# Kernel tuning notes

Measured on AMD Instinct MI355X. Metric: run time of the kernel, lower is better.

Reference implementation:

```python
import jax, jax.numpy as jnp
import numpy as np

D_MODEL = 1024
D_FF = 1024
NUM_EXPERTS = 8
TOP_K = 2


def setup_inputs() -> dict:
    key = jax.random.key(0)
    ks = jax.random.split(key, 5)
    s_in = 1.0 / np.sqrt(D_MODEL)
    s_ff = 1.0 / np.sqrt(D_FF)
    return {
        "x": jax.random.normal(ks[0], (4, 2048, D_MODEL), dtype=jnp.float32),
        "gate_w": jax.random.normal(ks[1], (NUM_EXPERTS, D_MODEL), dtype=jnp.float32) * s_in,
        # torch Linear weight layout: [out_features, in_features], stacked over experts
        "w_gate": jax.random.normal(ks[2], (NUM_EXPERTS, D_FF, D_MODEL), dtype=jnp.float32) * s_in,
        "w_up": jax.random.normal(ks[3], (NUM_EXPERTS, D_FF, D_MODEL), dtype=jnp.float32) * s_in,
        "w_down": jax.random.normal(ks[4], (NUM_EXPERTS, D_MODEL, D_FF), dtype=jnp.float32) * s_ff,
    }


def reference(x, gate_w, w_gate, w_up, w_down):
    B, S, D = x.shape
    T = B * S
    E = gate_w.shape[0]
    xt = x.reshape(T, D)

    # Router
    logits = xt @ gate_w.T                      # [T, E]
    probs = jax.nn.softmax(logits, axis=-1)
    top_v, top_i = jax.lax.top_k(probs, TOP_K)  # [T, K]
    top_v = top_v / jnp.sum(top_v, axis=-1, keepdims=True)

    tokens_per_expert = jnp.sum(jax.nn.one_hot(top_i, E, dtype=jnp.float32), axis=(0, 1))  # [E]
    f = tokens_per_expert / jnp.sum(tokens_per_expert)
    P = jnp.mean(probs, axis=0)
    aux_loss = E * jnp.sum(f * P)

    # Combine weights: per-token weight for each expert (sum over top-k slots)
    combine = jnp.zeros((T, E), dtype=x.dtype).at[jnp.arange(T)[:, None], top_i].add(top_v)  # [T, E]

    # Dense per-expert SwiGLU (equivalent math to masked gather/scatter loop)
    g = jnp.einsum('td,efd->etf', xt, w_gate)   # [E, T, F]
    u = jnp.einsum('td,efd->etf', xt, w_up)     # [E, T, F]
    act = jax.nn.silu(g) * u
    eo = jnp.einsum('etf,edf->etd', act, w_down)  # [E, T, D]

    out = jnp.einsum('te,etd->td', combine, eo).reshape(B, S, D)
    return out, aux_loss, tokens_per_expert
```

## Files before the change

kernel.cpp:

```cpp
#include <hip/hip_runtime.h>


#define T_TOK   8192
#define DM      1024
#define DFF     1024
#define NE      8
#define CAP     16384
#define R1_BLK  (T_TOK / 4)

typedef __attribute__((ext_vector_type(8))) short bf16x8;
typedef __attribute__((ext_vector_type(4))) float f32x4;

#define ASYNC16(gp, lp) __builtin_amdgcn_global_load_lds( \
    (const __attribute__((address_space(1))) unsigned int*)(gp), \
    (__attribute__((address_space(3))) unsigned int*)(lp), 16, 0, 0)

__device__ __forceinline__ unsigned short f2bf(float f) {
    union { float f; unsigned u; } c; c.f = f;
    unsigned r = c.u + 0x7fffu + ((c.u >> 16) & 1u);
    return (unsigned short)(r >> 16);
}

__global__ __launch_bounds__(256) void cvt_kernel(const float* __restrict__ src,
                                                  unsigned short* __restrict__ dst, int n) {
    int i = (blockIdx.x * 256 + threadIdx.x) * 4;
    if (i >= n) return;
    float4 v = *(const float4*)(src + i);
    ushort4 o;
    o.x = f2bf(v.x); o.y = f2bf(v.y); o.z = f2bf(v.z); o.w = f2bf(v.w);
    *(ushort4*)(dst + i) = o;
}

__global__ __launch_bounds__(256) void router_kernel(
    const float* __restrict__ x, const float* __restrict__ gate_w,
    unsigned short* __restrict__ xb,
    int* __restrict__ topi, float2* __restrict__ topw,
    float* __restrict__ psum_part)
{
    __shared__ float gw[NE * DM];
    __shared__ float blk_psum[NE];
    int tid = threadIdx.x;
    for (int i = tid; i < NE * DM; i += 256) gw[i] = gate_w[i];
    if (tid < NE) blk_psum[tid] = 0.f;
    __syncthreads();

    int wv = tid >> 6, lane = tid & 63;
    int t = blockIdx.x * 4 + wv;

    float acc[NE];
    #pragma unroll
    for (int e = 0; e < NE; ++e) acc[e] = 0.f;
    const float* xr = x + (size_t)t * DM;
    unsigned short* xbr = xb + (size_t)t * DM;
    #pragma unroll 4
    for (int i = 0; i < DM / 64; ++i) {
        float xv = xr[i * 64 + lane];
        xbr[i * 64 + lane] = f2bf(xv);
        #pragma unroll
        for (int e = 0; e < NE; ++e)
            acc[e] += xv * gw[e * DM + i * 64 + lane];
    }
    #pragma unroll
    for (int e = 0; e < NE; ++e) {
        float v = acc[e];
        #pragma unroll
        for (int s = 32; s > 0; s >>= 1) v += __shfl_xor(v, s, 64);
        acc[e] = v;
    }
    if (lane == 0) {
        float mx = acc[0];
        #pragma unroll
        for (int e = 1; e < NE; ++e) mx = fmaxf(mx, acc[e]);
        float p[NE], sum = 0.f;
        #pragma unroll
        for (int e = 0; e < NE; ++e) { p[e] = expf(acc[e] - mx); sum += p[e]; }
        float inv = 1.f / sum;
        #pragma unroll
        for (int e = 0; e < NE; ++e) { p[e] *= inv; atomicAdd(&blk_psum[e], p[e]); }
        int i1 = 0; float v1 = p[0];
        #pragma unroll
        for (int e = 1; e < NE; ++e) if (p[e] > v1) { v1 = p[e]; i1 = e; }
        int i2 = -1; float v2 = -1.f;
        #pragma unroll
        for (int e = 0; e < NE; ++e) { if (e == i1) continue; if (p[e] > v2) { v2 = p[e]; i2 = e; } }
        float winv = 1.f / (v1 + v2);
        topi[t] = i1 | (i2 << 8);
        topw[t] = make_float2(v1 * winv, v2 * winv);
    }
    __syncthreads();
    if (tid < NE) psum_part[blockIdx.x * NE + tid] = blk_psum[tid];
}

__global__ __launch_bounds__(256) void scatter_kernel(
    const int* __restrict__ topi, const float2* __restrict__ topw,
    int* __restrict__ elist, float* __restrict__ wlist, int* __restrict__ ecnt)
{
    __shared__ int lcnt[NE];
    __shared__ int lbase[NE];
    int tid = threadIdx.x;
    if (tid < NE) lcnt[tid] = 0;
    __syncthreads();
    int t = blockIdx.x * 256 + tid;
    int pk = topi[t];
    float2 w = topw[t];
    int e1 = pk & 0xff, e2 = (pk >> 8) & 0xff;
    int p1 = atomicAdd(&lcnt[e1], 1);
    int p2 = atomicAdd(&lcnt[e2], 1);
    __syncthreads();
    if (tid < NE) lbase[tid] = atomicAdd(&ecnt[tid], lcnt[tid]);
    __syncthreads();
    int o1 = lbase[e1] + p1;
    elist[e1 * CAP + o1] = t * 2 + 0;
    wlist[e1 * CAP + o1] = w.x;
    int o2 = lbase[e2] + p2;
    elist[e2 * CAP + o2] = t * 2 + 1;
    wlist[e2 * CAP + o2] = w.y;
}

__global__ __launch_bounds__(256) void finalize_kernel(
    const int* __restrict__ ecnt, const float* __restrict__ psum_part,
    float* __restrict__ out_tail)
{
    __shared__ float red[256];
    __shared__ float parts[NE];
    int tid = threadIdx.x;
    int e = tid & 7, b0 = tid >> 3;
    float s = 0.f;
    for (int b = b0; b < R1_BLK; b += 32) s += psum_part[b * NE + e];
    red[tid] = s;
    __syncthreads();
    if (tid < NE) {
        float tot = 0.f;
        #pragma unroll
        for (int j = 0; j < 32; ++j) tot += red[tid + NE * j];
        float P = tot / (float)T_TOK;
        float f = (float)ecnt[tid] / (float)(2 * T_TOK);
        parts[tid] = f * P;
        out_tail[1 + tid] = (float)ecnt[tid];
    }
    __syncthreads();
    if (tid == 0) {
        float s2 = 0.f;
        for (int i = 0; i < NE; ++i) s2 += parts[i];
        out_tail[0] = (float)NE * s2;
    }
}

__global__ __launch_bounds__(256) void gemm1_kernel(
    const unsigned short* __restrict__ xb,
    const unsigned short* __restrict__ wgb,
    const unsigned short* __restrict__ wub,
    const int* __restrict__ elist, const int* __restrict__ ecnt,
    unsigned short* __restrict__ Hbuf)
{
    int e = blockIdx.z, mt = blockIdx.y, ft = blockIdx.x;
    int ne = ecnt[e];
    if (mt * 128 >= ne) return;

    __shared__ unsigned short As[128 * 64];
    __shared__ unsigned short Gs[64 * 64];
    __shared__ unsigned short Us[64 * 64];
    __shared__ int tsafe[128];
    __shared__ int rawts[128];

    int tid = threadIdx.x;
    if (tid < 128) {
        int pos = mt * 128 + tid;
        int ts0 = elist[e * CAP + mt * 128];
        int ts = (pos < ne) ? elist[e * CAP + pos] : ts0;
        tsafe[tid] = ts >> 1;
        rawts[tid] = (pos < ne) ? ts : -1;
    }
    __syncthreads();

    int wave = tid >> 6, lane = tid & 63;
    int quad = lane >> 4, col = lane & 15;
    int cr = tid >> 3;
    int cl = ((tid & 7) ^ (cr & 7)) * 8;

    const size_t woff = (size_t)e * (size_t)DFF * DM;
    const unsigned short* ap[4];
    #pragma unroll
    for (int j = 0; j < 4; ++j) ap[j] = xb + (size_t)tsafe[j * 32 + cr] * DM + cl;
    const unsigned short* gp[2];
    const unsigned short* up[2];
    #pragma unroll
    for (int j = 0; j < 2; ++j) {
        gp[j] = wgb + woff + (size_t)(ft * 64 + j * 32 + cr) * DM + cl;
        up[j] = wub + woff + (size_t)(ft * 64 + j * 32 + cr) * DM + cl;
    }
    unsigned short* lA = As + wave * 512;
    unsigned short* lG = Gs + wave * 512;
    unsigned short* lU = Us + wave * 512;

    f32x4 accG[2][4], accU[2][4];
    #pragma unroll
    for (int i = 0; i < 2; ++i)
        #pragma unroll
        for (int n = 0; n < 4; ++n) { accG[i][n] = (f32x4){0,0,0,0}; accU[i][n] = (f32x4){0,0,0,0}; }

    for (int k0 = 0; k0 < DM; k0 += 64) {
        __syncthreads();
        #pragma unroll
        for (int j = 0; j < 4; ++j) ASYNC16(ap[j] + k0, lA + j * 2048);
        #pragma unroll
        for (int j = 0; j < 2; ++j) {
            ASYNC16(gp[j] + k0, lG + j * 2048);
            ASYNC16(up[j] + k0, lU + j * 2048);
        }
        __syncthreads();
        #pragma unroll
        for (int ksoff = 0; ksoff < 8; ksoff += 4) {
            bf16x8 a[2], g[4], u[4];
            #pragma unroll
            for (int i = 0; i < 2; ++i) {
                int m = wave * 32 + i * 16 + col;
                a[i] = *(const bf16x8*)&As[m * 64 + ((quad + ksoff) ^ (m & 7)) * 8];
            }
            #pragma unroll
            for (int n = 0; n < 4; ++n) {
                int nb = n * 16 + col;
                int off = nb * 64 + ((quad + ksoff) ^ (nb & 7)) * 8;
                g[n] = *(const bf16x8*)&Gs[off];
                u[n] = *(const bf16x8*)&Us[off];
            }
            #pragma unroll
            for (int i = 0; i < 2; ++i)
                #pragma unroll
                for (int n = 0; n < 4; ++n) {
                    accG[i][n] = __builtin_amdgcn_mfma_f32_16x16x32_bf16(a[i], g[n], accG[i][n], 0, 0, 0);
                    accU[i][n] = __builtin_amdgcn_mfma_f32_16x16x32_bf16(a[i], u[n], accU[i][n], 0, 0, 0);
                }
        }
    }
    #pragma unroll
    for (int i = 0; i < 2; ++i) {
        #pragma unroll
        for (int r = 0; r < 4; ++r) {
            int row = wave * 32 + i * 16 + quad * 4 + r;
            int ts = rawts[row];
            if (ts < 0) continue;
            unsigned short* hr = Hbuf + (size_t)ts * DFF + ft * 64 + col;
            #pragma unroll
            for (int n = 0; n < 4; ++n) {
                float gg = accG[i][n][r], uu = accU[i][n][r];
                float h = (gg / (1.f + expf(-gg))) * uu;
                hr[n * 16] = f2bf(h);
            }
        }
    }
}

__global__ __launch_bounds__(256) void gemm2_kernel(
    const unsigned short* __restrict__ Hbuf,
    const unsigned short* __restrict__ wdb,
    const int* __restrict__ elist, const float* __restrict__ wlist,
    const int* __restrict__ ecnt, float* __restrict__ out)
{
    int e = blockIdx.z, mt = blockIdx.y, dt = blockIdx.x;
    int ne = ecnt[e];
    if (mt * 128 >= ne) return;

    __shared__ unsigned short As[128 * 64];
    __shared__ unsigned short Bs[128 * 64];
    __shared__ int tsafe[128];
    __shared__ int rawts[128];
    __shared__ float wrow[128];

    int tid = threadIdx.x;
    if (tid < 128) {
        int pos = mt * 128 + tid;
        int ts0 = elist[e * CAP + mt * 128];
        int ts = (pos < ne) ? elist[e * CAP + pos] : ts0;
        tsafe[tid] = ts;
        rawts[tid] = (pos < ne) ? ts : -1;
        wrow[tid] = (pos < ne) ? wlist[e * CAP + pos] : 0.f;
    }
    __syncthreads();

    int wave = tid >> 6, lane = tid & 63;
    int quad = lane >> 4, col = lane & 15;
    int wr = (wave >> 1) * 64, wc = (wave & 1) * 64;
    int cr = tid >> 3;
    int cl = ((tid & 7) ^ (cr & 7)) * 8;

    const size_t woff = (size_t)e * (size_t)DM * DFF;
    const unsigned short* ap[4];
    const unsigned short* bp[4];
    #pragma unroll
    for (int j = 0; j < 4; ++j) {
        ap[j] = Hbuf + (size_t)tsafe[j * 32 + cr] * DFF + cl;
        bp[j] = wdb + woff + (size_t)(dt * 128 + j * 32 + cr) * DFF + cl;
    }
    unsigned short* lA = As + wave * 512;
    unsigned short* lB = Bs + wave * 512;

    f32x4 acc[4][4];
    #pragma unroll
    for (int i = 0; i < 4; ++i)
        #pragma unroll
        for (int n = 0; n < 4; ++n) acc[i][n] = (f32x4){0,0,0,0};

    for (int k0 = 0; k0 < DFF; k0 += 64) {
        __syncthreads();
        #pragma unroll
        for (int j = 0; j < 4; ++j) {
            ASYNC16(ap[j] + k0, lA + j * 2048);
            ASYNC16(bp[j] + k0, lB + j * 2048);
        }
        __syncthreads();
        #pragma unroll
        for (int ksoff = 0; ksoff < 8; ksoff += 4) {
            bf16x8 a[4], b[4];
            #pragma unroll
            for (int i = 0; i < 4; ++i) {
                int m = wr + i * 16 + col;
                a[i] = *(const bf16x8*)&As[m * 64 + ((quad + ksoff) ^ (m & 7)) * 8];
            }
            #pragma unroll
            for (int n = 0; n < 4; ++n) {
                int nb = wc + n * 16 + col;
                b[n] = *(const bf16x8*)&Bs[nb * 64 + ((quad + ksoff) ^ (nb & 7)) * 8];
            }
            #pragma unroll
            for (int i = 0; i < 4; ++i)
                #pragma unroll
                for (int n = 0; n < 4; ++n)
                    acc[i][n] = __builtin_amdgcn_mfma_f32_16x16x32_bf16(a[i], b[n], acc[i][n], 0, 0, 0);
        }
    }
    #pragma unroll
    for (int i = 0; i < 4; ++i) {
        #pragma unroll
        for (int r = 0; r < 4; ++r) {
            int row = wr + i * 16 + quad * 4 + r;
            int ts = rawts[row];
            if (ts < 0) continue;
            int t = ts >> 1;
            float w = wrow[row];
            float* orow = out + (size_t)t * DM + dt * 128 + wc + col;
            #pragma unroll
            for (int n = 0; n < 4; ++n)
                atomicAdd(orow + n * 16, w * acc[i][n][r]);
        }
    }
}

extern "C" void kernel_launch(void* const* d_in, const int* in_sizes, int n_in,
                              void* d_out, int out_size, void* d_ws, size_t ws_size,
                              hipStream_t stream) {
    const float* x      = (const float*)d_in[0];
    const float* gate_w = (const float*)d_in[1];
    const float* w_gate = (const float*)d_in[2];
    const float* w_up   = (const float*)d_in[3];
    const float* w_down = (const float*)d_in[4];
    float* out = (float*)d_out;

    char* p = (char*)d_ws;
    unsigned short* xb   = (unsigned short*)p; p += (size_t)T_TOK * DM * 2;
    unsigned short* wgb  = (unsigned short*)p; p += (size_t)NE * DFF * DM * 2;
    unsigned short* wub  = (unsigned short*)p; p += (size_t)NE * DFF * DM * 2;
    unsigned short* wdb  = (unsigned short*)p; p += (size_t)NE * DM * DFF * 2;
    unsigned short* Hbuf = (unsigned short*)p; p += (size_t)2 * T_TOK * DFF * 2;
    int*   elist = (int*)p;   p += (size_t)NE * CAP * 4;
    float* wlist = (float*)p; p += (size_t)NE * CAP * 4;
    int*   ecnt  = (int*)p;   p += NE * 4;
    int*   topi  = (int*)p;   p += (size_t)T_TOK * 4;
    float2* topw = (float2*)p; p += (size_t)T_TOK * 8;
    float* psum_part = (float*)p; p += (size_t)R1_BLK * NE * 4;

    hipMemsetAsync(d_out, 0, (size_t)out_size * 4, stream);
    hipMemsetAsync(ecnt, 0, NE * 4, stream);

    const int nW = NE * DFF * DM;
    cvt_kernel<<<(nW / 4 + 255) / 256, 256, 0, stream>>>(w_gate, wgb, nW);
    cvt_kernel<<<(nW / 4 + 255) / 256, 256, 0, stream>>>(w_up, wub, nW);
    cvt_kernel<<<(nW / 4 + 255) / 256, 256, 0, stream>>>(w_down, wdb, nW);

    router_kernel<<<R1_BLK, 256, 0, stream>>>(x, gate_w, xb, topi, topw, psum_part);
    scatter_kernel<<<T_TOK / 256, 256, 0, stream>>>(topi, topw, elist, wlist, ecnt);
    finalize_kernel<<<1, 256, 0, stream>>>(ecnt, psum_part, out + (size_t)T_TOK * DM);

    gemm1_kernel<<<dim3(DFF / 64, CAP / 128, NE), 256, 0, stream>>>(xb, wgb, wub, elist, ecnt, Hbuf);
    gemm2_kernel<<<dim3(DM / 128, CAP / 128, NE), 256, 0, stream>>>(Hbuf, wdb, elist, wlist, ecnt, out);
}
```

Measured before the change: 381.0 us.

## Replace atomic scatter-add in down-projection with bf16 staging and combine kernel

The down-projection GEMM now writes each token-slot's expert output as bf16 into a staging buffer (reusing the converted gate-weight buffer) instead of weighted float atomicAdds into the output. A new combine kernel reads both slots per token and writes the weighted sum directly, which also removes the output memset and the per-expert weight list. The three weight-conversion launches are merged into one kernel. This trades global atomic contention for an extra launch and a bf16 round-trip of expert outputs, which adds some precision loss.

```diff
diff --git a/kernel.cpp b/kernel.cpp
--- a/kernel.cpp
+++ b/kernel.cpp
@@ -20,15 +20,24 @@
     unsigned r = c.u + 0x7fffu + ((c.u >> 16) & 1u);
     return (unsigned short)(r >> 16);
 }
-
-__global__ __launch_bounds__(256) void cvt_kernel(const float* __restrict__ src,
-                                                  unsigned short* __restrict__ dst, int n) {
-    int i = (blockIdx.x * 256 + threadIdx.x) * 4;
-    if (i >= n) return;
-    float4 v = *(const float4*)(src + i);
+__device__ __forceinline__ float bf2f(unsigned short h) {
+    union { unsigned u; float f; } c; c.u = ((unsigned)h) << 16;
+    return c.f;
+}
+
+__global__ __launch_bounds__(256) void cvt3_kernel(
+    const float* __restrict__ s0, const float* __restrict__ s1, const float* __restrict__ s2,
+    unsigned short* __restrict__ d0, unsigned short* __restrict__ d1, unsigned short* __restrict__ d2)
+{
+    int idx = blockIdx.x * 256 + threadIdx.x;
+    int seg = idx >> 21;
+    int off = (idx & ((1 << 21) - 1)) * 4;
+    const float* s = (seg == 0) ? s0 : (seg == 1) ? s1 : s2;
+    unsigned short* d = (seg == 0) ? d0 : (seg == 1) ? d1 : d2;
+    float4 v = *(const float4*)(s + off);
     ushort4 o;
     o.x = f2bf(v.x); o.y = f2bf(v.y); o.z = f2bf(v.z); o.w = f2bf(v.w);
-    *(ushort4*)(dst + i) = o;
+    *(ushort4*)(d + off) = o;
 }
 
 __global__ __launch_bounds__(256) void router_kernel(
@@ -92,8 +101,8 @@
 }
 
 __global__ __launch_bounds__(256) void scatter_kernel(
-    const int* __restrict__ topi, const float2* __restrict__ topw,
-    int* __restrict__ elist, float* __restrict__ wlist, int* __restrict__ ecnt)
+    const int* __restrict__ topi,
+    int* __restrict__ elist, int* __restrict__ ecnt)
 {
     __shared__ int lcnt[NE];
     __shared__ int lbase[NE];
@@ -102,19 +111,14 @@
     __syncthreads();
     int t = blockIdx.x * 256 + tid;
     int pk = topi[t];
-    float2 w = topw[t];
     int e1 = pk & 0xff, e2 = (pk >> 8) & 0xff;
     int p1 = atomicAdd(&lcnt[e1], 1);
     int p2 = atomicAdd(&lcnt[e2], 1);
     __syncthreads();
     if (tid < NE) lbase[tid] = atomicAdd(&ecnt[tid], lcnt[tid]);
     __syncthreads();
-    int o1 = lbase[e1] + p1;
-    elist[e1 * CAP + o1] = t * 2 + 0;
-    wlist[e1 * CAP + o1] = w.x;
-    int o2 = lbase[e2] + p2;
-    elist[e2 * CAP + o2] = t * 2 + 1;
-    wlist[e2 * CAP + o2] = w.y;
+    elist[e1 * CAP + lbase[e1] + p1] = t * 2 + 0;
+    elist[e2 * CAP + lbase[e2] + p2] = t * 2 + 1;
 }
 
 __global__ __launch_bounds__(256) void finalize_kernel(
@@ -254,8 +258,8 @@
 __global__ __launch_bounds__(256) void gemm2_kernel(
     const unsigned short* __restrict__ Hbuf,
     const unsigned short* __restrict__ wdb,
-    const int* __restrict__ elist, const float* __restrict__ wlist,
-    const int* __restrict__ ecnt, float* __restrict__ out)
+    const int* __restrict__ elist, const int* __restrict__ ecnt,
+    unsigned short* __restrict__ eo)
 {
     int e = blockIdx.z, mt = blockIdx.y, dt = blockIdx.x;
     int ne = ecnt[e];
@@ -265,7 +269,6 @@
     __shared__ unsigned short Bs[128 * 64];
     __shared__ int tsafe[128];
     __shared__ int rawts[128];
-    __shared__ float wrow[128];
 
     int tid = threadIdx.x;
     if (tid < 128) {
@@ -274,7 +277,6 @@
         int ts = (pos < ne) ? elist[e * CAP + pos] : ts0;
         tsafe[tid] = ts;
         rawts[tid] = (pos < ne) ? ts : -1;
-        wrow[tid] = (pos < ne) ? wlist[e * CAP + pos] : 0.f;
     }
     __syncthreads();
 
@@ -336,14 +338,39 @@
             int row = wr + i * 16 + quad * 4 + r;
             int ts = rawts[row];
             if (ts < 0) continue;
-            int t = ts >> 1;
-            float w = wrow[row];
-            float* orow = out + (size_t)t * DM + dt * 128 + wc + col;
+            unsigned short* er = eo + (size_t)ts * DM + dt * 128 + wc + col;
             #pragma unroll
             for (int n = 0; n < 4; ++n)
-                atomicAdd(orow + n * 16, w * acc[i][n][r]);
-        }
-    }
+                er[n * 16] = f2bf(acc[i][n][r]);
+        }
+    }
+}
+
+__global__ __launch_bounds__(256) void combine_kernel(
+    const unsigned short* __restrict__ eo, const float2* __restrict__ topw,
+    float* __restrict__ out)
+{
+    int idx = blockIdx.x * 256 + threadIdx.x;
+    int t = idx >> 7;
+    int c = (idx & 127) << 3;
+    float2 w = topw[t];
+    const unsigned short* e0 = eo + (size_t)(t * 2) * DM + c;
+    ushort4 a0 = *(const ushort4*)e0;
+    ushort4 a1 = *(const ushort4*)(e0 + 4);
+    ushort4 b0 = *(const ushort4*)(e0 + DM);
+    ushort4 b1 = *(const ushort4*)(e0 + DM + 4);
+    float* orow = out + (size_t)t * DM + c;
+    float4 o0, o1;
+    o0.x = w.x * bf2f(a0.x) + w.y * bf2f(b0.x);
+    o0.y = w.x * bf2f(a0.y) + w.y * bf2f(b0.y);
+    o0.z = w.x * bf2f(a0.z) + w.y * bf2f(b0.z);
+    o0.w = w.x * bf2f(a0.w) + w.y * bf2f(b0.w);
+    o1.x = w.x * bf2f(a1.x) + w.y * bf2f(b1.x);
+    o1.y = w.x * bf2f(a1.y) + w.y * bf2f(b1.y);
+    o1.z = w.x * bf2f(a1.z) + w.y * bf2f(b1.z);
+    o1.w = w.x * bf2f(a1.w) + w.y * bf2f(b1.w);
+    *(float4*)orow = o0;
+    *(float4*)(orow + 4) = o1;
 }
 
 extern "C" void kernel_launch(void* const* d_in, const int* in_sizes, int n_in,
@@ -363,24 +390,22 @@
     unsigned short* wdb  = (unsigned short*)p; p += (size_t)NE * DM * DFF * 2;
     unsigned short* Hbuf = (unsigned short*)p; p += (size_t)2 * T_TOK * DFF * 2;
     int*   elist = (int*)p;   p += (size_t)NE * CAP * 4;
-    float* wlist = (float*)p; p += (size_t)NE * CAP * 4;
     int*   ecnt  = (int*)p;   p += NE * 4;
     int*   topi  = (int*)p;   p += (size_t)T_TOK * 4;
     float2* topw = (float2*)p; p += (size_t)T_TOK * 8;
     float* psum_part = (float*)p; p += (size_t)R1_BLK * NE * 4;
-
-    hipMemsetAsync(d_out, 0, (size_t)out_size * 4, stream);
+    unsigned short* eo = wgb;
+
     hipMemsetAsync(ecnt, 0, NE * 4, stream);
 
-    const int nW = NE * DFF * DM;
-    cvt_kernel<<<(nW / 4 + 255) / 256, 256, 0, stream>>>(w_gate, wgb, nW);
-    cvt_kernel<<<(nW / 4 + 255) / 256, 256, 0, stream>>>(w_up, wub, nW);
-    cvt_kernel<<<(nW / 4 + 255) / 256, 256, 0, stream>>>(w_down, wdb, nW);
+    cvt3_kernel<<<3 * (NE * DFF * DM / 4) / 256, 256, 0, stream>>>(
+        w_gate, w_up, w_down, wgb, wub, wdb);
 
     router_kernel<<<R1_BLK, 256, 0, stream>>>(x, gate_w, xb, topi, topw, psum_part);
-    scatter_kernel<<<T_TOK / 256, 256, 0, stream>>>(topi, topw, elist, wlist, ecnt);
+    scatter_kernel<<<T_TOK / 256, 256, 0, stream>>>(topi, elist, ecnt);
     finalize_kernel<<<1, 256, 0, stream>>>(ecnt, psum_part, out + (size_t)T_TOK * DM);
 
     gemm1_kernel<<<dim3(DFF / 64, CAP / 128, NE), 256, 0, stream>>>(xb, wgb, wub, elist, ecnt, Hbuf);
-    gemm2_kernel<<<dim3(DM / 128, CAP / 128, NE), 256, 0, stream>>>(Hbuf, wdb, elist, wlist, ecnt, out);
-}
+    gemm2_kernel<<<dim3(DM / 128, CAP / 128, NE), 256, 0, stream>>>(Hbuf, wdb, elist, ecnt, eo);
+    combine_kernel<<<T_TOK * DM / 8 / 256, 256, 0, stream>>>(eo, topw, out);
+}
```

Result: faster. 347.7 us (-8.7%).
